# Kernel optimization log

Measured on AMD Instinct MI355X. Metric: run time of the kernel, lower is better.

## Reference

```python
import jax, jax.numpy as jnp
import numpy as np

N_NODES = 40000
N_EDGES = 640000
D = 128


def setup_inputs() -> dict:
    key = jax.random.key(0)
    ks = jax.random.split(key, 7)
    x = jax.random.normal(ks[0], (N_NODES, D), dtype=jnp.float32)
    edge_index = jax.random.randint(ks[1], (2, N_EDGES), 0, N_NODES, dtype=jnp.int64)
    # uniform in [0.5, 1.5) to avoid division blow-up near zero
    edge_attr = jax.random.uniform(ks[2], (N_EDGES,), dtype=jnp.float32) + 0.5
    s = 1.0 / np.sqrt(D)
    W1 = jax.random.uniform(ks[3], (D, D), dtype=jnp.float32, minval=-s, maxval=s)
    b1 = jax.random.uniform(ks[4], (D,), dtype=jnp.float32, minval=-s, maxval=s)
    W2 = jax.random.uniform(ks[5], (D, D), dtype=jnp.float32, minval=-s, maxval=s)
    b2 = jax.random.uniform(ks[6], (D,), dtype=jnp.float32, minval=-s, maxval=s)
    return {"x": x, "edge_index": edge_index, "edge_attr": edge_attr,
            "W1": W1, "b1": b1, "W2": W2, "b2": b2}


def _layer(x, src, dst, edge_attr, W, b, num_nodes):
    # message: gather source features, divide by per-edge scalar
    msg = x[src] / edge_attr[:, None]                      # [E, D]
    # aggregate: scatter-add into destination nodes
    agg = jax.ops.segment_sum(msg, dst, num_segments=num_nodes)  # [N, D]
    # linear (torch: y = x @ W.T + b) then leaky_relu(0.01)
    y = agg @ W.T + b
    return jnp.where(y >= 0, y, 0.01 * y)


def reference(x, edge_index, edge_attr, W1, b1, W2, b2):
    src, dst = edge_index[0], edge_index[1]
    n = x.shape[0]
    x = jnp.maximum(_layer(x, src, dst, edge_attr, W1, b1, n), 0.0)
    x = jnp.maximum(_layer(x, src, dst, edge_attr, W2, b2, n), 0.0)
    return x
```

## Files before the change

### kernel.cpp

```cpp
#include <hip/hip_runtime.h>

#define D 128
#define CAP 64
typedef unsigned short u16;
typedef unsigned int   u32;

typedef __attribute__((ext_vector_type(8))) short short8;
typedef __attribute__((ext_vector_type(4))) float f32x4;

__device__ __forceinline__ u32 f2bf(float f) {
    u32 u = __float_as_uint(f);
    u += 0x7fffu + ((u >> 16) & 1u);
    return u >> 16;
}
__device__ __forceinline__ float2 bf2x2(u32 u) {
    float2 r;
    r.x = __uint_as_float(u << 16);
    r.y = __uint_as_float(u & 0xffff0000u);
    return r;
}

__global__ __launch_bounds__(256) void prep_kernel(
    const float4* __restrict__ x, uint2* __restrict__ xb,
    const float4* __restrict__ W1, const float4* __restrict__ W2,
    uint2* __restrict__ wb1, uint2* __restrict__ wb2,
    const int* __restrict__ src, const int* __restrict__ dst,
    const float* __restrict__ attr, int* __restrict__ counts,
    u32* __restrict__ combo, int E, int n4, int cvtb, int Nper, int N)
{
    const int bid = blockIdx.x;
    const int t   = threadIdx.x;

    if (bid < cvtb) {
        int i = bid * 256 + t;
        if (i < n4) {
            float4 v = x[i];
            uint2 o;
            o.x = f2bf(v.x) | (f2bf(v.y) << 16);
            o.y = f2bf(v.z) | (f2bf(v.w) << 16);
            xb[i] = o;
        }
    } else if (bid < cvtb + 32) {
        int i = (bid - cvtb) * 256 + t;
        const float4* in = (i < 4096) ? W1 : W2;
        uint2* out = (i < 4096) ? wb1 : wb2;
        int k = i & 4095;
        float4 v = in[k];
        uint2 o;
        o.x = f2bf(v.x) | (f2bf(v.y) << 16);
        o.y = f2bf(v.z) | (f2bf(v.w) << 16);
        out[k] = o;
    } else {
        const int sb    = bid - cvtb - 32;
        const int xcd   = sb & 7;
        const int chunk = sb >> 3;
        const int lo    = xcd * Nper;
        const int hi    = min(lo + Nper, N);
        long long e0 = (long long)chunk * 1024 + t * 4;

        if (e0 + 3 < E) {
            int4   s4 = *(const int4*)(src + e0);
            int4   d4 = *(const int4*)(dst + e0);
            float4 a4 = *(const float4*)(attr + e0);
            #pragma unroll
            for (int q = 0; q < 4; ++q) {
                int d = (q == 0) ? d4.x : (q == 1) ? d4.y : (q == 2) ? d4.z : d4.w;
                if (d >= lo && d < hi) {
                    int s = (q == 0) ? s4.x : (q == 1) ? s4.y : (q == 2) ? s4.z : s4.w;
                    float a = (q == 0) ? a4.x : (q == 1) ? a4.y : (q == 2) ? a4.z : a4.w;
                    int r = atomicAdd(&counts[d], 1);
                    if (r < CAP)
                        combo[((long long)d << 6) + r] =
                            (u32)s | (f2bf(1.0f / a) << 16);
                }
            }
        } else {
            for (int q = 0; q < 4; ++q) {
                long long e = e0 + q;
                if (e < E) {
                    int d = dst[e];
                    if (d >= lo && d < hi) {
                        int r = atomicAdd(&counts[d], 1);
                        if (r < CAP)
                            combo[((long long)d << 6) + r] =
                                (u32)src[e] | (f2bf(1.0f / attr[e]) << 16);
                    }
                }
            }
        }
    }
}

template <bool OUT_BF16>
__global__ __launch_bounds__(512, 8) void fused_layer_kernel(
    const u16* __restrict__ X, const u32* __restrict__ combo,
    const int* __restrict__ counts, const u16* __restrict__ Wb,
    const float* __restrict__ bias, void* __restrict__ Yv, int Nper, int N)
{
    __shared__ u16 As[32 * D];

    const int w    = threadIdx.x >> 6;
    const int lane = threadIdx.x & 63;
    const int g    = lane >> 4;
    const int c16  = lane & 15;

    const int xcd   = blockIdx.x & 7;
    const int slice = blockIdx.x >> 3;
    const int nl0   = slice * 32 + w * 4;
    const int nbase = xcd * Nper;

    int cnt4[4]; u32 ce4[4];
    #pragma unroll
    for (int i = 0; i < 4; ++i) {
        int nl = nl0 + i;
        bool v = (nl < Nper) && (nbase + nl < N);
        cnt4[i] = v ? min(counts[nbase + nl], CAP) : 0;
        ce4[i]  = v ? combo[((long long)(nbase + nl) << 6) + lane] : 0u;
    }

    #pragma unroll
    for (int i = 0; i < 4; ++i) {
        const int cnt = cnt4[i];
        const u32 ce  = ce4[i];
        float acc[8];
        #pragma unroll
        for (int c = 0; c < 8; ++c) acc[c] = 0.f;

        int j = 0;
        for (; j + 7 < cnt; j += 8) {
            u32 e0 = __shfl(ce, j + g);
            u32 e1 = __shfl(ce, j + 4 + g);
            uint4 r0 = *(const uint4*)(X + (long long)(e0 & 0xffffu) * D + c16 * 8);
            uint4 r1 = *(const uint4*)(X + (long long)(e1 & 0xffffu) * D + c16 * 8);
            float f0 = __uint_as_float(e0 & 0xffff0000u);
            float f1 = __uint_as_float(e1 & 0xffff0000u);
            float2 v;
            v = bf2x2(r0.x); acc[0] += v.x * f0; acc[1] += v.y * f0;
            v = bf2x2(r0.y); acc[2] += v.x * f0; acc[3] += v.y * f0;
            v = bf2x2(r0.z); acc[4] += v.x * f0; acc[5] += v.y * f0;
            v = bf2x2(r0.w); acc[6] += v.x * f0; acc[7] += v.y * f0;
            v = bf2x2(r1.x); acc[0] += v.x * f1; acc[1] += v.y * f1;
            v = bf2x2(r1.y); acc[2] += v.x * f1; acc[3] += v.y * f1;
            v = bf2x2(r1.z); acc[4] += v.x * f1; acc[5] += v.y * f1;
            v = bf2x2(r1.w); acc[6] += v.x * f1; acc[7] += v.y * f1;
        }
        for (; j + 3 < cnt; j += 4) {
            u32 e0 = __shfl(ce, j + g);
            uint4 r0 = *(const uint4*)(X + (long long)(e0 & 0xffffu) * D + c16 * 8);
            float f0 = __uint_as_float(e0 & 0xffff0000u);
            float2 v;
            v = bf2x2(r0.x); acc[0] += v.x * f0; acc[1] += v.y * f0;
            v = bf2x2(r0.y); acc[2] += v.x * f0; acc[3] += v.y * f0;
            v = bf2x2(r0.z); acc[4] += v.x * f0; acc[5] += v.y * f0;
            v = bf2x2(r0.w); acc[6] += v.x * f0; acc[7] += v.y * f0;
        }
        {
            int rem = cnt - j;
            u32 e0 = __shfl(ce, j + g);
            if (g < rem) {
                uint4 r0 = *(const uint4*)(X + (long long)(e0 & 0xffffu) * D + c16 * 8);
                float f0 = __uint_as_float(e0 & 0xffff0000u);
                float2 v;
                v = bf2x2(r0.x); acc[0] += v.x * f0; acc[1] += v.y * f0;
                v = bf2x2(r0.y); acc[2] += v.x * f0; acc[3] += v.y * f0;
                v = bf2x2(r0.z); acc[4] += v.x * f0; acc[5] += v.y * f0;
                v = bf2x2(r0.w); acc[6] += v.x * f0; acc[7] += v.y * f0;
            }
        }

        #pragma unroll
        for (int c = 0; c < 8; ++c) {
            acc[c] += __shfl_xor(acc[c], 16);
            acc[c] += __shfl_xor(acc[c], 32);
        }

        if (g == 0) {
            uint4 o;
            o.x = f2bf(acc[0]) | (f2bf(acc[1]) << 16);
            o.y = f2bf(acc[2]) | (f2bf(acc[3]) << 16);
            o.z = f2bf(acc[4]) | (f2bf(acc[5]) << 16);
            o.w = f2bf(acc[6]) | (f2bf(acc[7]) << 16);
            int row  = w * 4 + i;
            int slot = c16 ^ (row & 7);
            *(uint4*)&As[row * D + slot * 8] = o;
        }
    }

    __syncthreads();

    const int mrow = lane & 15;
    const int kq   = lane >> 4;
    const int h    = w >> 2;
    const int q    = w & 3;
    const int lr0  = h * 16;

    short8 afr[4];
    const u16* asrc = As + (lr0 + mrow) * D;
    #pragma unroll
    for (int ks = 0; ks < 4; ++ks)
        afr[ks] = *(const short8*)(asrc + ((kq + ks * 4) ^ (mrow & 7)) * 8);

    #pragma unroll
    for (int jn = 0; jn < 2; ++jn) {
        const int n0 = q * 32 + jn * 16;
        float bv = bias[n0 + mrow];
        f32x4 acc2 = {bv, bv, bv, bv};
        const u16* wrow = Wb + (long long)(n0 + mrow) * D + kq * 8;
        #pragma unroll
        for (int ks = 0; ks < 4; ++ks) {
            short8 bfr = *(const short8*)(wrow + ks * 32);
            acc2 = __builtin_amdgcn_mfma_f32_16x16x32_bf16(afr[ks], bfr, acc2, 0, 0, 0);
        }
        #pragma unroll
        for (int r = 0; r < 4; ++r) {
            float v = acc2[r] > 0.f ? acc2[r] : 0.f;
            int row = lr0 + kq * 4 + r;
            int nl  = slice * 32 + row;
            if (nl < Nper && nbase + nl < N) {
                long long off = (long long)(nbase + nl) * D + n0 + mrow;
                if (OUT_BF16)
                    *((u16*)Yv + off) = (u16)f2bf(v);
                else
                    *((float*)Yv + off) = v;
            }
        }
    }
}

extern "C" void kernel_launch(void* const* d_in, const int* in_sizes, int n_in,
                              void* d_out, int out_size, void* d_ws, size_t ws_size,
                              hipStream_t stream)
{
    const float* x    = (const float*)d_in[0];
    const int*   eidx = (const int*)d_in[1];
    const float* attr = (const float*)d_in[2];
    const float* W1   = (const float*)d_in[3];
    const float* b1   = (const float*)d_in[4];
    const float* W2   = (const float*)d_in[5];
    const float* b2   = (const float*)d_in[6];

    const int N = in_sizes[0] / D;
    const int E = in_sizes[2];
    const int* src = eidx;
    const int* dst = eidx + E;
    const int Nper = (N + 7) / 8;

    char* p = (char*)d_ws;
    u16*  xb    = (u16*)p;   p += ((size_t)N * D * 2 + 15) & ~15ULL;
    u16*  aggB  = (u16*)p;   p += ((size_t)N * D * 2 + 15) & ~15ULL;
    u32*  combo = (u32*)p;   p += (size_t)N * CAP * 4;
    u16*  wb1   = (u16*)p;   p += (size_t)D * D * 2;
    u16*  wb2   = (u16*)p;   p += (size_t)D * D * 2;
    int*  counts= (int*)p;

    const int n4    = N * D / 4;
    const int cvtb  = (n4 + 255) / 256;
    const int hfb   = 8 * ((E + 1023) / 1024);
    const int prepb = cvtb + 32 + hfb;
    const int fusedb = 8 * ((Nper + 31) / 32);

    hipMemsetAsync(counts, 0, (size_t)N * 4, stream);
    prep_kernel<<<prepb, 256, 0, stream>>>(
        (const float4*)x, (uint2*)xb, (const float4*)W1, (const float4*)W2,
        (uint2*)wb1, (uint2*)wb2, src, dst, attr, counts,
        combo, E, n4, cvtb, Nper, N);

    fused_layer_kernel<true><<<fusedb, 512, 0, stream>>>(
        xb, combo, counts, wb1, b1, aggB, Nper, N);
    fused_layer_kernel<false><<<fusedb, 512, 0, stream>>>(
        aggB, combo, counts, wb2, b2, d_out, Nper, N);
}
```

Measured before the change: 184.7 us.

## Split features into two column planes and gather each half in separate passes

Node features are stored as two 64-column bf16 planes, and each layer's gather runs in two passes. The first pass aggregates plane 0 into a workspace buffer. The second gathers plane 1 into shared memory and then runs the MFMA GEMM, taking its A fragments from both the buffer and LDS. The aim is to halve the gathered working set per pass so it fits better in cache and the random row gathers hit more often. In exchange it adds a kernel launch per layer, a round-trip of half the aggregate through global memory, and 8-byte rather than 16-byte gather loads.

```diff
diff --git a/kernel.cpp b/kernel.cpp
--- a/kernel.cpp
+++ b/kernel.cpp
@@ -21,7 +21,7 @@
 }
 
 __global__ __launch_bounds__(256) void prep_kernel(
-    const float4* __restrict__ x, uint2* __restrict__ xb,
+    const float4* __restrict__ x, uint2* __restrict__ xp0, uint2* __restrict__ xp1,
     const float4* __restrict__ W1, const float4* __restrict__ W2,
     uint2* __restrict__ wb1, uint2* __restrict__ wb2,
     const int* __restrict__ src, const int* __restrict__ dst,
@@ -38,7 +38,10 @@
             uint2 o;
             o.x = f2bf(v.x) | (f2bf(v.y) << 16);
             o.y = f2bf(v.z) | (f2bf(v.w) << 16);
-            xb[i] = o;
+            int r  = i >> 5;
+            int q4 = i & 31;
+            uint2* pl = (q4 < 16) ? xp0 : xp1;
+            pl[r * 16 + (q4 & 15)] = o;
         }
     } else if (bid < cvtb + 32) {
         int i = (bid - cvtb) * 256 + t;
@@ -91,14 +94,10 @@
     }
 }
 
-template <bool OUT_BF16>
-__global__ __launch_bounds__(512, 8) void fused_layer_kernel(
-    const u16* __restrict__ X, const u32* __restrict__ combo,
-    const int* __restrict__ counts, const u16* __restrict__ Wb,
-    const float* __restrict__ bias, void* __restrict__ Yv, int Nper, int N)
+__global__ __launch_bounds__(512) void gather_half_kernel(
+    const u16* __restrict__ Xp, const u32* __restrict__ combo,
+    const int* __restrict__ counts, u16* __restrict__ AggP, int Nper, int N)
 {
-    __shared__ u16 As[32 * D];
-
     const int w    = threadIdx.x >> 6;
     const int lane = threadIdx.x & 63;
     const int g    = lane >> 4;
@@ -122,67 +121,139 @@
     for (int i = 0; i < 4; ++i) {
         const int cnt = cnt4[i];
         const u32 ce  = ce4[i];
-        float acc[8];
-        #pragma unroll
-        for (int c = 0; c < 8; ++c) acc[c] = 0.f;
+        float a0 = 0.f, a1 = 0.f, a2 = 0.f, a3 = 0.f;
 
         int j = 0;
         for (; j + 7 < cnt; j += 8) {
             u32 e0 = __shfl(ce, j + g);
             u32 e1 = __shfl(ce, j + 4 + g);
-            uint4 r0 = *(const uint4*)(X + (long long)(e0 & 0xffffu) * D + c16 * 8);
-            uint4 r1 = *(const uint4*)(X + (long long)(e1 & 0xffffu) * D + c16 * 8);
+            uint2 r0 = *(const uint2*)(Xp + (long long)(e0 & 0xffffu) * 64 + c16 * 4);
+            uint2 r1 = *(const uint2*)(Xp + (long long)(e1 & 0xffffu) * 64 + c16 * 4);
             float f0 = __uint_as_float(e0 & 0xffff0000u);
             float f1 = __uint_as_float(e1 & 0xffff0000u);
             float2 v;
-            v = bf2x2(r0.x); acc[0] += v.x * f0; acc[1] += v.y * f0;
-            v = bf2x2(r0.y); acc[2] += v.x * f0; acc[3] += v.y * f0;
-            v = bf2x2(r0.z); acc[4] += v.x * f0; acc[5] += v.y * f0;
-            v = bf2x2(r0.w); acc[6] += v.x * f0; acc[7] += v.y * f0;
-            v = bf2x2(r1.x); acc[0] += v.x * f1; acc[1] += v.y * f1;
-            v = bf2x2(r1.y); acc[2] += v.x * f1; acc[3] += v.y * f1;
-            v = bf2x2(r1.z); acc[4] += v.x * f1; acc[5] += v.y * f1;
-            v = bf2x2(r1.w); acc[6] += v.x * f1; acc[7] += v.y * f1;
+            v = bf2x2(r0.x); a0 += v.x * f0; a1 += v.y * f0;
+            v = bf2x2(r0.y); a2 += v.x * f0; a3 += v.y * f0;
+            v = bf2x2(r1.x); a0 += v.x * f1; a1 += v.y * f1;
+            v = bf2x2(r1.y); a2 += v.x * f1; a3 += v.y * f1;
         }
         for (; j + 3 < cnt; j += 4) {
             u32 e0 = __shfl(ce, j + g);
-            uint4 r0 = *(const uint4*)(X + (long long)(e0 & 0xffffu) * D + c16 * 8);
+            uint2 r0 = *(const uint2*)(Xp + (long long)(e0 & 0xffffu) * 64 + c16 * 4);
             float f0 = __uint_as_float(e0 & 0xffff0000u);
             float2 v;
-            v = bf2x2(r0.x); acc[0] += v.x * f0; acc[1] += v.y * f0;
-            v = bf2x2(r0.y); acc[2] += v.x * f0; acc[3] += v.y * f0;
-            v = bf2x2(r0.z); acc[4] += v.x * f0; acc[5] += v.y * f0;
-            v = bf2x2(r0.w); acc[6] += v.x * f0; acc[7] += v.y * f0;
+            v = bf2x2(r0.x); a0 += v.x * f0; a1 += v.y * f0;
+            v = bf2x2(r0.y); a2 += v.x * f0; a3 += v.y * f0;
         }
         {
             int rem = cnt - j;
             u32 e0 = __shfl(ce, j + g);
             if (g < rem) {
-                uint4 r0 = *(const uint4*)(X + (long long)(e0 & 0xffffu) * D + c16 * 8);
+                uint2 r0 = *(const uint2*)(Xp + (long long)(e0 & 0xffffu) * 64 + c16 * 4);
                 float f0 = __uint_as_float(e0 & 0xffff0000u);
                 float2 v;
-                v = bf2x2(r0.x); acc[0] += v.x * f0; acc[1] += v.y * f0;
-                v = bf2x2(r0.y); acc[2] += v.x * f0; acc[3] += v.y * f0;
-                v = bf2x2(r0.z); acc[4] += v.x * f0; acc[5] += v.y * f0;
-                v = bf2x2(r0.w); acc[6] += v.x * f0; acc[7] += v.y * f0;
-            }
-        }
-
-        #pragma unroll
-        for (int c = 0; c < 8; ++c) {
-            acc[c] += __shfl_xor(acc[c], 16);
-            acc[c] += __shfl_xor(acc[c], 32);
-        }
+                v = bf2x2(r0.x); a0 += v.x * f0; a1 += v.y * f0;
+                v = bf2x2(r0.y); a2 += v.x * f0; a3 += v.y * f0;
+            }
+        }
+
+        a0 += __shfl_xor(a0, 16); a0 += __shfl_xor(a0, 32);
+        a1 += __shfl_xor(a1, 16); a1 += __shfl_xor(a1, 32);
+        a2 += __shfl_xor(a2, 16); a2 += __shfl_xor(a2, 32);
+        a3 += __shfl_xor(a3, 16); a3 += __shfl_xor(a3, 32);
 
         if (g == 0) {
-            uint4 o;
-            o.x = f2bf(acc[0]) | (f2bf(acc[1]) << 16);
-            o.y = f2bf(acc[2]) | (f2bf(acc[3]) << 16);
-            o.z = f2bf(acc[4]) | (f2bf(acc[5]) << 16);
-            o.w = f2bf(acc[6]) | (f2bf(acc[7]) << 16);
-            int row  = w * 4 + i;
-            int slot = c16 ^ (row & 7);
-            *(uint4*)&As[row * D + slot * 8] = o;
+            int nl = nl0 + i;
+            if (nl < Nper && nbase + nl < N) {
+                uint2 o;
+                o.x = f2bf(a0) | (f2bf(a1) << 16);
+                o.y = f2bf(a2) | (f2bf(a3) << 16);
+                *(uint2*)(AggP + (long long)(nbase + nl) * 64 + c16 * 4) = o;
+            }
+        }
+    }
+}
+
+template <bool OUT_BF16>
+__global__ __launch_bounds__(512) void gather_gemm_kernel(
+    const u16* __restrict__ Xp, const u16* __restrict__ Agg0,
+    const u32* __restrict__ combo, const int* __restrict__ counts,
+    const u16* __restrict__ Wb, const float* __restrict__ bias,
+    void* __restrict__ Y0, void* __restrict__ Y1, int Nper, int N)
+{
+    __shared__ u16 As[32 * 64];
+
+    const int w    = threadIdx.x >> 6;
+    const int lane = threadIdx.x & 63;
+    const int g    = lane >> 4;
+    const int c16  = lane & 15;
+
+    const int xcd   = blockIdx.x & 7;
+    const int slice = blockIdx.x >> 3;
+    const int nl0   = slice * 32 + w * 4;
+    const int nbase = xcd * Nper;
+
+    int cnt4[4]; u32 ce4[4];
+    #pragma unroll
+    for (int i = 0; i < 4; ++i) {
+        int nl = nl0 + i;
+        bool v = (nl < Nper) && (nbase + nl < N);
+        cnt4[i] = v ? min(counts[nbase + nl], CAP) : 0;
+        ce4[i]  = v ? combo[((long long)(nbase + nl) << 6) + lane] : 0u;
+    }
+
+    #pragma unroll
+    for (int i = 0; i < 4; ++i) {
+        const int cnt = cnt4[i];
+        const u32 ce  = ce4[i];
+        float a0 = 0.f, a1 = 0.f, a2 = 0.f, a3 = 0.f;
+
+        int j = 0;
+        for (; j + 7 < cnt; j += 8) {
+            u32 e0 = __shfl(ce, j + g);
+            u32 e1 = __shfl(ce, j + 4 + g);
+            uint2 r0 = *(const uint2*)(Xp + (long long)(e0 & 0xffffu) * 64 + c16 * 4);
+            uint2 r1 = *(const uint2*)(Xp + (long long)(e1 & 0xffffu) * 64 + c16 * 4);
+            float f0 = __uint_as_float(e0 & 0xffff0000u);
+            float f1 = __uint_as_float(e1 & 0xffff0000u);
+            float2 v;
+            v = bf2x2(r0.x); a0 += v.x * f0; a1 += v.y * f0;
+            v = bf2x2(r0.y); a2 += v.x * f0; a3 += v.y * f0;
+            v = bf2x2(r1.x); a0 += v.x * f1; a1 += v.y * f1;
+            v = bf2x2(r1.y); a2 += v.x * f1; a3 += v.y * f1;
+        }
+        for (; j + 3 < cnt; j += 4) {
+            u32 e0 = __shfl(ce, j + g);
+            uint2 r0 = *(const uint2*)(Xp + (long long)(e0 & 0xffffu) * 64 + c16 * 4);
+            float f0 = __uint_as_float(e0 & 0xffff0000u);
+            float2 v;
+            v = bf2x2(r0.x); a0 += v.x * f0; a1 += v.y * f0;
+            v = bf2x2(r0.y); a2 += v.x * f0; a3 += v.y * f0;
+        }
+        {
+            int rem = cnt - j;
+            u32 e0 = __shfl(ce, j + g);
+            if (g < rem) {
+                uint2 r0 = *(const uint2*)(Xp + (long long)(e0 & 0xffffu) * 64 + c16 * 4);
+                float f0 = __uint_as_float(e0 & 0xffff0000u);
+                float2 v;
+                v = bf2x2(r0.x); a0 += v.x * f0; a1 += v.y * f0;
+                v = bf2x2(r0.y); a2 += v.x * f0; a3 += v.y * f0;
+            }
+        }
+
+        a0 += __shfl_xor(a0, 16); a0 += __shfl_xor(a0, 32);
+        a1 += __shfl_xor(a1, 16); a1 += __shfl_xor(a1, 32);
+        a2 += __shfl_xor(a2, 16); a2 += __shfl_xor(a2, 32);
+        a3 += __shfl_xor(a3, 16); a3 += __shfl_xor(a3, 32);
+
+        if (g == 0) {
+            uint2 o;
+            o.x = f2bf(a0) | (f2bf(a1) << 16);
+            o.y = f2bf(a2) | (f2bf(a3) << 16);
+            int row = w * 4 + i;
+            int s   = (c16 >> 1) ^ (row & 7);
+            *(uint2*)&As[row * 64 + s * 8 + (c16 & 1) * 4] = o;
         }
     }
 
@@ -194,11 +265,17 @@
     const int q    = w & 3;
     const int lr0  = h * 16;
 
+    const int lrowA = lr0 + mrow;
+    const int nlAc  = min(slice * 32 + lrowA, Nper - 1);
+    const u16* arow0 = Agg0 + (long long)(nbase + nlAc) * 64 + kq * 8;
+
     short8 afr[4];
-    const u16* asrc = As + (lr0 + mrow) * D;
-    #pragma unroll
-    for (int ks = 0; ks < 4; ++ks)
-        afr[ks] = *(const short8*)(asrc + ((kq + ks * 4) ^ (mrow & 7)) * 8);
+    afr[0] = *(const short8*)(arow0);
+    afr[1] = *(const short8*)(arow0 + 32);
+    const u16* asrc = As + lrowA * 64;
+    #pragma unroll
+    for (int ks = 0; ks < 2; ++ks)
+        afr[2 + ks] = *(const short8*)(asrc + ((ks * 4 + kq) ^ (lrowA & 7)) * 8);
 
     #pragma unroll
     for (int jn = 0; jn < 2; ++jn) {
@@ -214,14 +291,17 @@
         #pragma unroll
         for (int r = 0; r < 4; ++r) {
             float v = acc2[r] > 0.f ? acc2[r] : 0.f;
-            int row = lr0 + kq * 4 + r;
-            int nl  = slice * 32 + row;
+            int lrow = lr0 + kq * 4 + r;
+            int nl   = slice * 32 + lrow;
             if (nl < Nper && nbase + nl < N) {
-                long long off = (long long)(nbase + nl) * D + n0 + mrow;
-                if (OUT_BF16)
-                    *((u16*)Yv + off) = (u16)f2bf(v);
-                else
-                    *((float*)Yv + off) = v;
+                long long gnode = nbase + nl;
+                int col = n0 + mrow;
+                if (OUT_BF16) {
+                    u16* yp = (col < 64) ? (u16*)Y0 : (u16*)Y1;
+                    yp[gnode * 64 + (col & 63)] = (u16)f2bf(v);
+                } else {
+                    ((float*)Y0)[gnode * D + col] = v;
+                }
             }
         }
     }
@@ -245,9 +325,13 @@
     const int* dst = eidx + E;
     const int Nper = (N + 7) / 8;
 
+    const size_t planeB = (size_t)N * 64 * 2;
     char* p = (char*)d_ws;
-    u16*  xb    = (u16*)p;   p += ((size_t)N * D * 2 + 15) & ~15ULL;
-    u16*  aggB  = (u16*)p;   p += ((size_t)N * D * 2 + 15) & ~15ULL;
+    u16*  xp0   = (u16*)p;   p += planeB;
+    u16*  xp1   = (u16*)p;   p += planeB;
+    u16*  yp0   = (u16*)p;   p += planeB;
+    u16*  yp1   = (u16*)p;   p += planeB;
+    u16*  ag0   = (u16*)p;   p += planeB;
     u32*  combo = (u32*)p;   p += (size_t)N * CAP * 4;
     u16*  wb1   = (u16*)p;   p += (size_t)D * D * 2;
     u16*  wb2   = (u16*)p;   p += (size_t)D * D * 2;
@@ -257,16 +341,20 @@
     const int cvtb  = (n4 + 255) / 256;
     const int hfb   = 8 * ((E + 1023) / 1024);
     const int prepb = cvtb + 32 + hfb;
-    const int fusedb = 8 * ((Nper + 31) / 32);
+    const int gatherb = 8 * ((Nper + 31) / 32);
 
     hipMemsetAsync(counts, 0, (size_t)N * 4, stream);
     prep_kernel<<<prepb, 256, 0, stream>>>(
-        (const float4*)x, (uint2*)xb, (const float4*)W1, (const float4*)W2,
+        (const float4*)x, (uint2*)xp0, (uint2*)xp1,
+        (const float4*)W1, (const float4*)W2,
         (uint2*)wb1, (uint2*)wb2, src, dst, attr, counts,
         combo, E, n4, cvtb, Nper, N);
 
-    fused_layer_kernel<true><<<fusedb, 512, 0, stream>>>(
-        xb, combo, counts, wb1, b1, aggB, Nper, N);
-    fused_layer_kernel<false><<<fusedb, 512, 0, stream>>>(
-        aggB, combo, counts, wb2, b2, d_out, Nper, N);
-}
+    gather_half_kernel<<<gatherb, 512, 0, stream>>>(xp0, combo, counts, ag0, Nper, N);
+    gather_gemm_kernel<true><<<gatherb, 512, 0, stream>>>(
+        xp1, ag0, combo, counts, wb1, b1, yp0, yp1, Nper, N);
+
+    gather_half_kernel<<<gatherb, 512, 0, stream>>>(yp0, combo, counts, ag0, Nper, N);
+    gather_gemm_kernel<false><<<gatherb, 512, 0, stream>>>(
+        yp1, ag0, combo, counts, wb2, b2, d_out, nullptr, Nper, N);
+}
```

After: 212.4 us. +15.0%, slower.
